# Performance work log

Measured on AMD Instinct MI355X. Metric: run time of the kernel, lower is better.

Reference implementation:

```python
import jax, jax.numpy as jnp
import numpy as np

N_NODES = 50000
N_EDGES = 800000
IN_CH = 256
HID = 256
OUT_CH = 128


def setup_inputs() -> dict:
    key = jax.random.key(0)
    ks = jax.random.split(key, 12)
    x = jax.random.normal(ks[0], (N_NODES, IN_CH), dtype=jnp.float32)
    adj_rows = jnp.sort(jax.random.randint(ks[1], (N_EDGES,), 0, N_NODES, dtype=jnp.int32))
    adj_cols = jax.random.randint(ks[2], (N_EDGES,), 0, N_NODES, dtype=jnp.int32)
    # normalized adjacency weights (~1/degree scale)
    adj_vals = jax.random.uniform(ks[3], (N_EDGES,), dtype=jnp.float32) / 16.0
    def xavier(k, fan_in, fan_out):
        lim = float(np.sqrt(6.0 / (fan_in + fan_out)))
        return jax.random.uniform(k, (fan_in, fan_out), dtype=jnp.float32, minval=-lim, maxval=lim)
    Wa0 = xavier(ks[4], IN_CH, HID)
    Wa1 = xavier(ks[5], HID, HID)
    Wl0 = xavier(ks[6], IN_CH + HID, HID)
    Wl1 = xavier(ks[7], 2 * HID, OUT_CH)
    return {
        'x': x, 'adj_rows': adj_rows, 'adj_cols': adj_cols, 'adj_vals': adj_vals,
        'Wa0': Wa0, 'ba0': jnp.zeros((HID,), jnp.float32),
        'Wa1': Wa1, 'ba1': jnp.zeros((HID,), jnp.float32),
        'Wl0': Wl0, 'bl0': jnp.zeros((HID,), jnp.float32),
        'Wl1': Wl1, 'bl1': jnp.zeros((OUT_CH,), jnp.float32),
    }


def reference(x, adj_rows, adj_cols, adj_vals, Wa0, ba0, Wa1, ba1, Wl0, bl0, Wl1, bl1):
    n = x.shape[0]

    def spmm(h):
        # sparse adj @ h : gather neighbor rows, scale by edge weight, segment-sum into dst
        return jax.ops.segment_sum(adj_vals[:, None] * h[adj_cols], adj_rows, num_segments=n)

    # layer 0
    agg = jax.nn.relu(spmm(x) @ Wa0 + ba0)
    h = jax.nn.relu(jnp.concatenate((x, agg), axis=1) @ Wl0 + bl0)
    # layer 1 (last: no activation after linear)
    agg = jax.nn.relu(spmm(h) @ Wa1 + ba1)
    h = jnp.concatenate((h, agg), axis=1) @ Wl1 + bl1
    # F.normalize: row-wise L2 with eps=1e-12
    norm = jnp.maximum(jnp.linalg.norm(h, axis=1, keepdims=True), 1e-12)
    return h / norm
```

## Files before the change

### kernel.cpp

```cpp
#include <hip/hip_runtime.h>

typedef unsigned short u16;
typedef __attribute__((ext_vector_type(8))) __bf16 bf16x8;
typedef __attribute__((ext_vector_type(4))) float f32x4;
typedef __attribute__((ext_vector_type(8))) u16 u16x8;
typedef __attribute__((ext_vector_type(4))) u16 u16x4;

__device__ __forceinline__ float bf2f(u16 u) {
  return __builtin_bit_cast(float, ((unsigned)u) << 16);
}
__device__ __forceinline__ u16 f2bf(float f) {
  unsigned x = __builtin_bit_cast(unsigned, f);
  x += 0x7fffu + ((x >> 16) & 1u);
  return (u16)(x >> 16);
}
__device__ __forceinline__ f32x4 cvt4(u16x4 v) {
  return (f32x4){bf2f(v.x), bf2f(v.y), bf2f(v.z), bf2f(v.w)};
}
__device__ __forceinline__ void gload_lds16(const void* g, void* l) {
  __builtin_amdgcn_global_load_lds(
      (const __attribute__((address_space(1))) void*)g,
      (__attribute__((address_space(3))) void*)l, 16, 0, 0);
}

__global__ void prep_kernel(const float* __restrict__ x, u16* __restrict__ x_bf, int cvtxBlocks,
                            const float* __restrict__ W0, u16* __restrict__ T0,
                            const float* __restrict__ W1, u16* __restrict__ T1,
                            const float* __restrict__ W2, u16* __restrict__ T2,
                            const float* __restrict__ W3, u16* __restrict__ T3,
                            const int* __restrict__ rows, int nE, int* __restrict__ rp, int nN) {
  int b = blockIdx.x;
  if (b < cvtxBlocks) {
    int i = b * 256 + threadIdx.x;
    if (i >= nN * 64) return;
    const float4 v = ((const float4*)x)[i];
    u16x4 o = { f2bf(v.x), f2bf(v.y), f2bf(v.z), f2bf(v.w) };
    ((u16x4*)x_bf)[i] = o;
    return;
  }
  b -= cvtxBlocks;
  if (b < 1280) {
    int i = b * 256 + threadIdx.x;
    const float* W; u16* T; int K, N;
    if (i < 65536)        { W = W0; T = T0; K = 256; N = 256; }
    else if (i < 131072)  { W = W1; T = T1; K = 256; N = 256; i -= 65536; }
    else if (i < 262144)  { W = W2; T = T2; K = 512; N = 256; i -= 131072; }
    else if (i < 327680)  { W = W3; T = T3; K = 512; N = 128; i -= 262144; }
    else return;
    int k = i / N, n = i - k * N;
    T[(size_t)n * K + k] = f2bf(W[i]);
    return;
  }
  b -= 1280;
  int i = b * 256 + threadIdx.x;
  if (i > nN) return;
  int lo = 0, hi = nE;
  while (lo < hi) { int mid = (lo + hi) >> 1; if (rows[mid] < i) lo = mid + 1; else hi = mid; }
  rp[i] = lo;
}

__global__ __launch_bounds__(128) void spmm_kernel(
    const u16* __restrict__ X, const int* __restrict__ rp,
    const int* __restrict__ cols, const float* __restrict__ vals,
    u16* __restrict__ out, int nN) {
  int lane = threadIdx.x & 63;
  int node = blockIdx.x * 2 + (threadIdx.x >> 6);
  if (node >= nN) return;
  int e0 = rp[node], e1 = rp[node + 1];
  f32x4 s0 = {0.f, 0.f, 0.f, 0.f}, s1 = s0, s2 = s0, s3 = s0;
  const u16* xp = X + (size_t)lane * 4;
  int e = e0;
  for (; e + 8 <= e1; e += 8) {
    int c[8]; float v[8]; u16x4 xv[8];
    #pragma unroll
    for (int i = 0; i < 8; ++i) { c[i] = cols[e + i]; v[i] = vals[e + i]; }
    #pragma unroll
    for (int i = 0; i < 8; ++i) xv[i] = *(const u16x4*)(xp + (size_t)c[i] * 256);
    s0 += v[0] * cvt4(xv[0]); s1 += v[1] * cvt4(xv[1]);
    s2 += v[2] * cvt4(xv[2]); s3 += v[3] * cvt4(xv[3]);
    s0 += v[4] * cvt4(xv[4]); s1 += v[5] * cvt4(xv[5]);
    s2 += v[6] * cvt4(xv[6]); s3 += v[7] * cvt4(xv[7]);
  }
  if (e + 4 <= e1) {
    int c0 = cols[e], c1 = cols[e + 1], c2 = cols[e + 2], c3 = cols[e + 3];
    float v0 = vals[e], v1 = vals[e + 1], v2 = vals[e + 2], v3 = vals[e + 3];
    u16x4 x0 = *(const u16x4*)(xp + (size_t)c0 * 256);
    u16x4 x1 = *(const u16x4*)(xp + (size_t)c1 * 256);
    u16x4 x2 = *(const u16x4*)(xp + (size_t)c2 * 256);
    u16x4 x3 = *(const u16x4*)(xp + (size_t)c3 * 256);
    s0 += v0 * cvt4(x0); s1 += v1 * cvt4(x1);
    s2 += v2 * cvt4(x2); s3 += v3 * cvt4(x3);
    e += 4;
  }
  for (; e < e1; ++e) {
    int c = cols[e];
    float v = vals[e];
    s0 += v * cvt4(*(const u16x4*)(xp + (size_t)c * 256));
  }
  f32x4 s = (s0 + s1) + (s2 + s3);
  u16x4 o = { f2bf(s.x), f2bf(s.y), f2bf(s.z), f2bf(s.w) };
  *(u16x4*)(out + (size_t)node * 256 + lane * 4) = o;
}

template<int N2, bool NORM>
__global__ __launch_bounds__(256) void fused_kernel(
    const u16* __restrict__ agg, const u16* __restrict__ xh,
    const u16* __restrict__ W1t, const float* __restrict__ b1,
    const u16* __restrict__ W2t, const float* __restrict__ b2,
    void* __restrict__ outp, int M) {
  constexpr int NI2 = N2 / 32;
  __shared__ u16 As[64 * 32];
  __shared__ u16 Bs[256 * 32];
  __shared__ u16 Ag[64 * 256];
  __shared__ float red[64][2];

  const int tid = threadIdx.x;
  const int lane = tid & 63;
  const int wid = tid >> 6;
  const int wr = wid >> 1, wc = wid & 1;
  const int row0b = blockIdx.x * 64;
  const int lr = lane & 15, kg = lane >> 4;

  auto stageA = [&](const u16* src, int kt) {
    const int row = tid >> 2, ksd = tid & 3;
    const int kss = ksd ^ ((row >> 1) & 3);
    int grow = row0b + row; if (grow >= M) grow = M - 1;
    gload_lds16(src + (size_t)grow * 256 + kt * 32 + kss * 8, &As[tid * 8]);
  };
  auto stageB1 = [&](int kt) {
    #pragma unroll
    for (int i = 0; i < 4; ++i) {
      const int u = i * 256 + tid;
      const int col = u >> 2, ksd = u & 3;
      const int kss = ksd ^ ((col >> 1) & 3);
      gload_lds16(W1t + (size_t)col * 256 + kt * 32 + kss * 8, &Bs[u * 8]);
    }
  };
  auto stageB2 = [&](int kt) {
    #pragma unroll
    for (int i = 0; i < N2 / 64; ++i) {
      const int u = i * 256 + tid;
      const int col = u >> 2, ksd = u & 3;
      const int kss = ksd ^ ((col >> 1) & 3);
      gload_lds16(W2t + (size_t)col * 512 + kt * 32 + kss * 8, &Bs[u * 8]);
    }
  };

  f32x4 acc[2][8];

  #pragma unroll
  for (int ni = 0; ni < 8; ++ni) {
    float bv = b1[wc * 128 + ni * 16 + lr];
    acc[0][ni] = (f32x4){bv, bv, bv, bv};
    acc[1][ni] = acc[0][ni];
  }
  for (int kt = 0; kt < 8; ++kt) {
    if (kt) __syncthreads();
    stageB1(kt);
    stageA(agg, kt);
    __syncthreads();
    bf16x8 a[2], b[8];
    #pragma unroll
    for (int mi = 0; mi < 2; ++mi) {
      const int r = wr * 32 + mi * 16 + lr;
      a[mi] = __builtin_bit_cast(bf16x8,
          *(const u16x8*)&As[r * 32 + ((kg ^ ((r >> 1) & 3)) << 3)]);
    }
    #pragma unroll
    for (int ni = 0; ni < 8; ++ni) {
      const int cb = wc * 128 + ni * 16 + lr;
      b[ni] = __builtin_bit_cast(bf16x8,
          *(const u16x8*)&Bs[cb * 32 + ((kg ^ ((cb >> 1) & 3)) << 3)]);
    }
    #pragma unroll
    for (int mi = 0; mi < 2; ++mi)
      #pragma unroll
      for (int ni = 0; ni < 8; ++ni)
        acc[mi][ni] = __builtin_amdgcn_mfma_f32_16x16x32_bf16(a[mi], b[ni], acc[mi][ni], 0, 0, 0);
  }
  #pragma unroll
  for (int mi = 0; mi < 2; ++mi)
    #pragma unroll
    for (int j = 0; j < 4; ++j) {
      const int rl = wr * 32 + mi * 16 + kg * 4 + j;
      #pragma unroll
      for (int ni = 0; ni < 8; ++ni) {
        float v = acc[mi][ni][j];
        v = v > 0.f ? v : 0.f;
        const int c = wc * 128 + ni * 16 + lr;
        Ag[rl * 256 + (c >> 6) * 64 + ((((c >> 3) & 7) ^ (rl & 7)) << 3) + (c & 7)] = f2bf(v);
      }
    }
  __syncthreads();

  #pragma unroll
  for (int ni = 0; ni < NI2; ++ni) {
    float bv = b2[wc * (N2 / 2) + ni * 16 + lr];
    acc[0][ni] = (f32x4){bv, bv, bv, bv};
    acc[1][ni] = acc[0][ni];
  }
  for (int kt = 0; kt < 16; ++kt) {
    if (kt) __syncthreads();
    stageB2(kt);
    if (kt < 8) stageA(xh, kt);
    __syncthreads();
    bf16x8 a[2], b[NI2];
    if (kt < 8) {
      #pragma unroll
      for (int mi = 0; mi < 2; ++mi) {
        const int r = wr * 32 + mi * 16 + lr;
        a[mi] = __builtin_bit_cast(bf16x8,
            *(const u16x8*)&As[r * 32 + ((kg ^ ((r >> 1) & 3)) << 3)]);
      }
    } else {
      const int w64 = (kt - 8) >> 1;
      const int q8 = ((kt - 8) & 1) * 4 + kg;
      #pragma unroll
      for (int mi = 0; mi < 2; ++mi) {
        const int r = wr * 32 + mi * 16 + lr;
        a[mi] = __builtin_bit_cast(bf16x8,
            *(const u16x8*)&Ag[r * 256 + w64 * 64 + ((q8 ^ (r & 7)) << 3)]);
      }
    }
    #pragma unroll
    for (int ni = 0; ni < NI2; ++ni) {
      const int cb = wc * (N2 / 2) + ni * 16 + lr;
      b[ni] = __builtin_bit_cast(bf16x8,
          *(const u16x8*)&Bs[cb * 32 + ((kg ^ ((cb >> 1) & 3)) << 3)]);
    }
    #pragma unroll
    for (int mi = 0; mi < 2; ++mi)
      #pragma unroll
      for (int ni = 0; ni < NI2; ++ni)
        acc[mi][ni] = __builtin_amdgcn_mfma_f32_16x16x32_bf16(a[mi], b[ni], acc[mi][ni], 0, 0, 0);
  }

  float invn[2][4];
  if (NORM) {
    #pragma unroll
    for (int mi = 0; mi < 2; ++mi)
      #pragma unroll
      for (int j = 0; j < 4; ++j) {
        float p = 0.f;
        #pragma unroll
        for (int ni = 0; ni < NI2; ++ni) { float v = acc[mi][ni][j]; p += v * v; }
        #pragma unroll
        for (int m = 1; m < 16; m <<= 1) p += __shfl_xor(p, m, 64);
        int rl = wr * 32 + mi * 16 + kg * 4 + j;
        if (lr == 0) red[rl][wc] = p;
      }
    __syncthreads();
    #pragma unroll
    for (int mi = 0; mi < 2; ++mi)
      #pragma unroll
      for (int j = 0; j < 4; ++j) {
        int rl = wr * 32 + mi * 16 + kg * 4 + j;
        float ss = red[rl][0] + red[rl][1];
        float nrm = sqrtf(ss);
        nrm = nrm > 1e-12f ? nrm : 1e-12f;
        invn[mi][j] = 1.f / nrm;
      }
  }

  #pragma unroll
  for (int mi = 0; mi < 2; ++mi)
    #pragma unroll
    for (int j = 0; j < 4; ++j) {
      int r = row0b + wr * 32 + mi * 16 + kg * 4 + j;
      if (r >= M) continue;
      #pragma unroll
      for (int ni = 0; ni < NI2; ++ni) {
        float v = acc[mi][ni][j];
        int c = wc * (N2 / 2) + ni * 16 + lr;
        if (NORM) {
          ((float*)outp)[(size_t)r * N2 + c] = v * invn[mi][j];
        } else {
          v = v > 0.f ? v : 0.f;
          ((u16*)outp)[(size_t)r * N2 + c] = f2bf(v);
        }
      }
    }
}

extern "C" void kernel_launch(void* const* d_in, const int* in_sizes, int n_in,
                              void* d_out, int out_size, void* d_ws, size_t ws_size,
                              hipStream_t stream) {
  const float* x        = (const float*)d_in[0];
  const int*   adj_rows = (const int*)d_in[1];
  const int*   adj_cols = (const int*)d_in[2];
  const float* adj_vals = (const float*)d_in[3];
  const float* Wa0 = (const float*)d_in[4];
  const float* ba0 = (const float*)d_in[5];
  const float* Wa1 = (const float*)d_in[6];
  const float* ba1 = (const float*)d_in[7];
  const float* Wl0 = (const float*)d_in[8];
  const float* bl0 = (const float*)d_in[9];
  const float* Wl1 = (const float*)d_in[10];
  const float* bl1 = (const float*)d_in[11];

  const int nN = in_sizes[0] / 256;
  const int nE = in_sizes[1];

  char* ws = (char*)d_ws;
  size_t off = 0;
  auto alloc = [&](size_t bytes) -> void* {
    void* p = ws + off;
    off += (bytes + 255) & ~(size_t)255;
    return p;
  };
  u16* x_bf  = (u16*)alloc((size_t)nN * 256 * 2);
  u16* aggA  = (u16*)alloc((size_t)nN * 256 * 2);
  u16* h_bf  = (u16*)alloc((size_t)nN * 256 * 2);
  int* rp    = (int*)alloc((size_t)(nN + 1) * 4);
  u16* wt_a0 = (u16*)alloc(256 * 256 * 2);
  u16* wt_a1 = (u16*)alloc(256 * 256 * 2);
  u16* wt_l0 = (u16*)alloc(512 * 256 * 2);
  u16* wt_l1 = (u16*)alloc(512 * 128 * 2);
  if (off > ws_size) return;

  dim3 blk(256);
  const int cvtxBlocks = (nN * 64 + 255) / 256;
  const int rpBlocks = (nN + 1 + 255) / 256;
  prep_kernel<<<dim3(cvtxBlocks + 1280 + rpBlocks), blk, 0, stream>>>(
      x, x_bf, cvtxBlocks, Wa0, wt_a0, Wa1, wt_a1, Wl0, wt_l0, Wl1, wt_l1,
      adj_rows, nE, rp, nN);

  const int MB = (nN + 63) / 64;
  dim3 gF(MB);
  dim3 gNode((nN + 1) / 2);
  dim3 sblk(128);

  spmm_kernel<<<gNode, sblk, 0, stream>>>(x_bf, rp, adj_cols, adj_vals, aggA, nN);
  fused_kernel<256, false><<<gF, blk, 0, stream>>>(aggA, x_bf, wt_a0, ba0, wt_l0, bl0, h_bf, nN);
  spmm_kernel<<<gNode, sblk, 0, stream>>>(h_bf, rp, adj_cols, adj_vals, aggA, nN);
  fused_kernel<128, true><<<gF, blk, 0, stream>>>(aggA, h_bf, wt_a1, ba1, wt_l1, bl1, (float*)d_out, nN);
}
```

Before: 215.3 us.

## Double-buffer LDS tiles in fused GEMM with async prefetch and vmcnt waits

Adds a second LDS buffer for the A and B tiles in both GEMM phases of the fused kernel. The next k-tile is prefetched with global_load_lds while the current tile feeds the MFMAs. Raw s_barrier plus explicit s_waitcnt vmcnt counts replace __syncthreads, so only the older loads are waited on. This is meant to hide global load latency, but it doubles the As/Bs LDS footprint, which may lower occupancy, and hand-counted vmcnt values are fragile.

```diff
diff --git a/kernel.cpp b/kernel.cpp
--- a/kernel.cpp
+++ b/kernel.cpp
@@ -21,6 +21,16 @@
   __builtin_amdgcn_global_load_lds(
       (const __attribute__((address_space(1))) void*)g,
       (__attribute__((address_space(3))) void*)l, 16, 0, 0);
+}
+__device__ __forceinline__ void barrier_raw() {
+  asm volatile("s_barrier" ::: "memory");
+}
+template<int N> __device__ __forceinline__ void waitv() {
+  if constexpr (N == 0) asm volatile("s_waitcnt vmcnt(0)" ::: "memory");
+  else if constexpr (N == 2) asm volatile("s_waitcnt vmcnt(2)" ::: "memory");
+  else if constexpr (N == 3) asm volatile("s_waitcnt vmcnt(3)" ::: "memory");
+  else if constexpr (N == 4) asm volatile("s_waitcnt vmcnt(4)" ::: "memory");
+  else if constexpr (N == 5) asm volatile("s_waitcnt vmcnt(5)" ::: "memory");
 }
 
 __global__ void prep_kernel(const float* __restrict__ x, u16* __restrict__ x_bf, int cvtxBlocks,
@@ -109,8 +119,9 @@
     const u16* __restrict__ W2t, const float* __restrict__ b2,
     void* __restrict__ outp, int M) {
   constexpr int NI2 = N2 / 32;
-  __shared__ u16 As[64 * 32];
-  __shared__ u16 Bs[256 * 32];
+  constexpr int NB2 = N2 / 64;
+  __shared__ u16 As[2][64 * 32];
+  __shared__ u16 Bs[2][256 * 32];
   __shared__ u16 Ag[64 * 256];
   __shared__ float red[64][2];
 
@@ -121,28 +132,18 @@
   const int row0b = blockIdx.x * 64;
   const int lr = lane & 15, kg = lane >> 4;
 
-  auto stageA = [&](const u16* src, int kt) {
+  auto stageA = [&](const u16* src, int kt, int buf) {
     const int row = tid >> 2, ksd = tid & 3;
     const int kss = ksd ^ ((row >> 1) & 3);
     int grow = row0b + row; if (grow >= M) grow = M - 1;
-    gload_lds16(src + (size_t)grow * 256 + kt * 32 + kss * 8, &As[tid * 8]);
+    gload_lds16(src + (size_t)grow * 256 + kt * 32 + kss * 8, &As[buf][tid * 8]);
   };
-  auto stageB1 = [&](int kt) {
-    #pragma unroll
-    for (int i = 0; i < 4; ++i) {
+  auto stageB = [&](const u16* Wt, int KW, int NC, int kt, int buf) {
+    for (int i = 0; i < NC / 64; ++i) {
       const int u = i * 256 + tid;
       const int col = u >> 2, ksd = u & 3;
       const int kss = ksd ^ ((col >> 1) & 3);
-      gload_lds16(W1t + (size_t)col * 256 + kt * 32 + kss * 8, &Bs[u * 8]);
-    }
-  };
-  auto stageB2 = [&](int kt) {
-    #pragma unroll
-    for (int i = 0; i < N2 / 64; ++i) {
-      const int u = i * 256 + tid;
-      const int col = u >> 2, ksd = u & 3;
-      const int kss = ksd ^ ((col >> 1) & 3);
-      gload_lds16(W2t + (size_t)col * 512 + kt * 32 + kss * 8, &Bs[u * 8]);
+      gload_lds16(Wt + (size_t)col * KW + kt * 32 + kss * 8, &Bs[buf][u * 8]);
     }
   };
 
@@ -154,29 +155,35 @@
     acc[0][ni] = (f32x4){bv, bv, bv, bv};
     acc[1][ni] = acc[0][ni];
   }
+  stageA(agg, 0, 0); stageB(W1t, 256, 256, 0, 0);
   for (int kt = 0; kt < 8; ++kt) {
-    if (kt) __syncthreads();
-    stageB1(kt);
-    stageA(agg, kt);
-    __syncthreads();
+    const int cur = kt & 1;
+    if (kt < 7) {
+      stageA(agg, kt + 1, cur ^ 1); stageB(W1t, 256, 256, kt + 1, cur ^ 1);
+      waitv<5>();
+    } else {
+      waitv<0>();
+    }
+    barrier_raw();
     bf16x8 a[2], b[8];
     #pragma unroll
     for (int mi = 0; mi < 2; ++mi) {
       const int r = wr * 32 + mi * 16 + lr;
       a[mi] = __builtin_bit_cast(bf16x8,
-          *(const u16x8*)&As[r * 32 + ((kg ^ ((r >> 1) & 3)) << 3)]);
+          *(const u16x8*)&As[cur][r * 32 + ((kg ^ ((r >> 1) & 3)) << 3)]);
     }
     #pragma unroll
     for (int ni = 0; ni < 8; ++ni) {
       const int cb = wc * 128 + ni * 16 + lr;
       b[ni] = __builtin_bit_cast(bf16x8,
-          *(const u16x8*)&Bs[cb * 32 + ((kg ^ ((cb >> 1) & 3)) << 3)]);
+          *(const u16x8*)&Bs[cur][cb * 32 + ((kg ^ ((cb >> 1) & 3)) << 3)]);
     }
     #pragma unroll
     for (int mi = 0; mi < 2; ++mi)
       #pragma unroll
       for (int ni = 0; ni < 8; ++ni)
         acc[mi][ni] = __builtin_amdgcn_mfma_f32_16x16x32_bf16(a[mi], b[ni], acc[mi][ni], 0, 0, 0);
+    barrier_raw();
   }
   #pragma unroll
   for (int mi = 0; mi < 2; ++mi)
@@ -199,18 +206,24 @@
     acc[0][ni] = (f32x4){bv, bv, bv, bv};
     acc[1][ni] = acc[0][ni];
   }
+  stageB(W2t, 512, N2, 0, 0); stageA(xh, 0, 0);
   for (int kt = 0; kt < 16; ++kt) {
-    if (kt) __syncthreads();
-    stageB2(kt);
-    if (kt < 8) stageA(xh, kt);
-    __syncthreads();
+    const int cur = kt & 1;
+    if (kt < 15) {
+      stageB(W2t, 512, N2, kt + 1, cur ^ 1);
+      if (kt + 1 < 8) { stageA(xh, kt + 1, cur ^ 1); waitv<NB2 + 1>(); }
+      else waitv<NB2>();
+    } else {
+      waitv<0>();
+    }
+    barrier_raw();
     bf16x8 a[2], b[NI2];
     if (kt < 8) {
       #pragma unroll
       for (int mi = 0; mi < 2; ++mi) {
         const int r = wr * 32 + mi * 16 + lr;
         a[mi] = __builtin_bit_cast(bf16x8,
-            *(const u16x8*)&As[r * 32 + ((kg ^ ((r >> 1) & 3)) << 3)]);
+            *(const u16x8*)&As[cur][r * 32 + ((kg ^ ((r >> 1) & 3)) << 3)]);
       }
     } else {
       const int w64 = (kt - 8) >> 1;
@@ -226,13 +239,14 @@
     for (int ni = 0; ni < NI2; ++ni) {
       const int cb = wc * (N2 / 2) + ni * 16 + lr;
       b[ni] = __builtin_bit_cast(bf16x8,
-          *(const u16x8*)&Bs[cb * 32 + ((kg ^ ((cb >> 1) & 3)) << 3)]);
+          *(const u16x8*)&Bs[cur][cb * 32 + ((kg ^ ((cb >> 1) & 3)) << 3)]);
     }
     #pragma unroll
     for (int mi = 0; mi < 2; ++mi)
       #pragma unroll
       for (int ni = 0; ni < NI2; ++ni)
         acc[mi][ni] = __builtin_amdgcn_mfma_f32_16x16x32_bf16(a[mi], b[ni], acc[mi][ni], 0, 0, 0);
+    barrier_raw();
   }
 
   float invn[2][4];
```

After: 208.8 us. 3.0% less time.
